# Kernel tuning notes

Measured on AMD Instinct MI355X. Metric: run time of the kernel, lower is better.

## Reference

```python
import jax, jax.numpy as jnp
import numpy as np

IN_CH, OUT_CH = 32, 32
MODES1, MODES2 = 16, 16
B, H, W = 16, 256, 256


def setup_inputs() -> dict:
    key = jax.random.key(0)
    k1, k2, k3 = jax.random.split(key, 3)
    scale = 1.0 / (IN_CH * OUT_CH)
    x = jax.random.normal(k1, (B, IN_CH, H, W), dtype=jnp.float32)
    # weights stored as real view of complex: [..., 2] = (real, imag)
    w1 = scale * jax.random.uniform(k2, (IN_CH, OUT_CH, MODES1, MODES2, 2), dtype=jnp.float32)
    w2 = scale * jax.random.uniform(k3, (IN_CH, OUT_CH, MODES1, MODES2, 2), dtype=jnp.float32)
    return {"x": x, "w1": w1, "w2": w2}


def reference(x, w1, w2):
    m1, m2 = MODES1, MODES2
    b, _, h, w = x.shape
    x_ft = jnp.fft.rfft2(x, axes=(-2, -1))  # [B, in_ch, H, W//2+1] complex
    c1 = w1[..., 0] + 1j * w1[..., 1]       # [in_ch, out_ch, m1, m2]
    c2 = w2[..., 0] + 1j * w2[..., 1]
    o1 = jnp.einsum('bixy,ioxy->boxy', x_ft[:, :, :m1, :m2], c1)
    o2 = jnp.einsum('bixy,ioxy->boxy', x_ft[:, :, -m1:, :m2], c2)
    out_ft = jnp.zeros((b, c1.shape[1], h, w // 2 + 1), dtype=x_ft.dtype)
    out_ft = out_ft.at[:, :, :m1, :m2].set(o1)
    out_ft = out_ft.at[:, :, -m1:, :m2].set(o2)
    return jnp.fft.irfft2(out_ft, s=(h, w), axes=(-2, -1))
```

## Files before the change

kernel.cpp:

```cpp
#include <hip/hip_runtime.h>
#include <math.h>

#define BB 16
#define CC 32
#define HH 256
#define WW 256
#define NIMG (BB * CC)

typedef _Float16 f16;
typedef __attribute__((ext_vector_type(8))) _Float16 f16x8;
typedef __attribute__((ext_vector_type(4))) float f32x4;

constexpr float TWO_PI_OVER_256 = 6.28318530717958647692f / 256.0f;

#define N_TWF 8192
#define N_ACOL 32768
#define N_AINV 16384
#define N_BINV 8192

static __device__ __forceinline__ f32x4 mfma3(f16x8 ah, f16x8 al, f16x8 bh,
                                              f16x8 bl, f32x4 c) {
  c = __builtin_amdgcn_mfma_f32_16x16x32_f16(ah, bh, c, 0, 0, 0);
  c = __builtin_amdgcn_mfma_f32_16x16x32_f16(ah, bl, c, 0, 0, 0);
  c = __builtin_amdgcn_mfma_f32_16x16x32_f16(al, bh, c, 0, 0, 0);
  return c;
}

static __device__ __forceinline__ void split16(float v, f16* hi, f16* lo) {
  f16 h_ = (f16)v;
  *hi = h_;
  *lo = (f16)(v - (float)h_);
}

__global__ __launch_bounds__(256) void k_tw(f16* __restrict__ fb) {
  const int id = blockIdx.x * 256 + threadIdx.x;
  f16* twf_hi = fb;
  f16* twf_lo = twf_hi + N_TWF;
  f16* acol_hi = twf_lo + N_TWF;
  f16* acol_lo = acol_hi + N_ACOL;
  f16* ainv_hi = acol_lo + N_ACOL;
  f16* ainv_lo = ainv_hi + N_AINV;
  f16* binv_hi = ainv_lo + N_AINV;
  f16* binv_lo = binv_hi + N_BINV;

  float v;
  f16 *dh, *dl;
  if (id < N_TWF) {
    int idx = id;
    int j = idx & 7, lane = (idx >> 3) & 63, ks = (idx >> 9) & 7,
        nt = (idx >> 12) & 1;
    int col = nt * 16 + (lane & 15);
    int w = ks * 32 + ((lane >> 4) << 3) + j;
    int kx = col >> 1, ri = col & 1;
    int ph = (kx * w) & 255;
    float s, c;
    sincosf(TWO_PI_OVER_256 * (float)ph, &s, &c);
    v = ri ? -s : c;
    dh = twf_hi + idx;
    dl = twf_lo + idx;
  } else if (id < N_TWF + N_ACOL) {
    int idx = id - N_TWF;
    int j = idx & 7, lane = (idx >> 3) & 63, ks = (idx >> 9) & 15,
        mt = (idx >> 13) & 3;
    int row = mt * 16 + (lane & 15);
    int k = ks * 32 + ((lane >> 4) << 3) + j;
    int h = k >> 1, rj = k & 1;
    int zr = (row < 32) ? row : row - 32;
    int ky = (zr < 16) ? zr : 224 + zr;
    int ph = (ky * h) & 255;
    float s, c;
    sincosf(TWO_PI_OVER_256 * (float)ph, &s, &c);
    if (row < 32)
      v = rj ? s : c;
    else
      v = rj ? c : -s;
    dh = acol_hi + idx;
    dl = acol_lo + idx;
  } else if (id < N_TWF + N_ACOL + N_AINV) {
    int idx = id - N_TWF - N_ACOL;
    int j = idx & 7, lane = (idx >> 3) & 63, ks = (idx >> 9) & 1,
        mt = (idx >> 10) & 15;
    int h = mt * 16 + (lane & 15);
    int k = ks * 32 + ((lane >> 4) << 3) + j;
    int zr = k >> 1, rj = k & 1;
    int ky = (zr < 16) ? zr : 224 + zr;
    int ph = (ky * h) & 255;
    float s, c;
    sincosf(TWO_PI_OVER_256 * (float)ph, &s, &c);
    v = rj ? s : c;
    dh = ainv_hi + idx;
    dl = ainv_lo + idx;
  } else {
    int idx = id - N_TWF - N_ACOL - N_AINV;
    int j = idx & 7, lane = (idx >> 3) & 63, nt = (idx >> 9) & 15;
    int w = nt * 16 + (lane & 15);
    int k = ((lane >> 4) << 3) + j;
    int kx = k >> 1, ri = k & 1;
    int ph = (kx * w) & 255;
    float s, c;
    sincosf(TWO_PI_OVER_256 * (float)ph, &s, &c);
    float scale = ((kx == 0) ? 1.0f : 2.0f) / 65536.0f;
    v = ri ? -scale * s : scale * c;
    dh = binv_hi + idx;
    dl = binv_lo + idx;
  }
  f16 hi, lo;
  split16(v, &hi, &lo);
  *dh = hi;
  *dl = lo;
}

__global__ __launch_bounds__(256) void k_fwd(const float* __restrict__ x,
                                             const f16* __restrict__ twf_hi,
                                             const f16* __restrict__ twf_lo,
                                             const f16* __restrict__ acol_hi,
                                             const f16* __restrict__ acol_lo,
                                             float* __restrict__ Z) {
  __shared__ __align__(16) f16 Yc_hi[16 * 520];
  __shared__ __align__(16) f16 Yc_lo[16 * 520];
  const int t = threadIdx.x, lane = t & 63, wid = t >> 6;
  const int l15 = lane & 15, kgrp = lane >> 4;
  const int img = blockIdx.x;
  const float* xim = x + (size_t)img * (HH * WW);

  for (int r = 0; r < 4; ++r) {
    const int mt = r * 4 + wid;
    f32x4 acc0 = {0.f, 0.f, 0.f, 0.f}, acc1 = {0.f, 0.f, 0.f, 0.f};
    const float* ap = xim + (mt * 16 + l15) * WW + kgrp * 8;
#pragma unroll
    for (int ks = 0; ks < 8; ++ks) {
      float4 v0 = *(const float4*)(ap + ks * 32);
      float4 v1 = *(const float4*)(ap + ks * 32 + 4);
      float vv[8] = {v0.x, v0.y, v0.z, v0.w, v1.x, v1.y, v1.z, v1.w};
      f16x8 ah, al;
#pragma unroll
      for (int e = 0; e < 8; ++e) {
        f16 h_ = (f16)vv[e];
        ah[e] = h_;
        al[e] = (f16)(vv[e] - (float)h_);
      }
      const int b0 = ((0 * 8 + ks) * 64 + lane) * 8;
      const int b1 = ((1 * 8 + ks) * 64 + lane) * 8;
      f16x8 b0h = *(const f16x8*)(twf_hi + b0);
      f16x8 b0l = *(const f16x8*)(twf_lo + b0);
      f16x8 b1h = *(const f16x8*)(twf_hi + b1);
      f16x8 b1l = *(const f16x8*)(twf_lo + b1);
      acc0 = mfma3(ah, al, b0h, b0l, acc0);
      acc1 = mfma3(ah, al, b1h, b1l, acc1);
    }
#pragma unroll
    for (int nt = 0; nt < 2; ++nt) {
#pragma unroll
      for (int jj = 0; jj < 4; ++jj) {
        const int h = mt * 16 + kgrp * 4 + jj;
        const int n = nt * 16 + l15;
        const int kx = n >> 1, ri = n & 1;
        float v = (nt == 0) ? acc0[jj] : acc1[jj];
        f16 hv = (f16)v;
        Yc_hi[kx * 520 + 2 * h + ri] = hv;
        Yc_lo[kx * 520 + 2 * h + ri] = (f16)(v - (float)hv);
      }
    }
  }
  __syncthreads();
  f32x4 zacc = {0.f, 0.f, 0.f, 0.f};
#pragma unroll 4
  for (int ks = 0; ks < 16; ++ks) {
    const int ao = ((wid * 16 + ks) * 64 + lane) * 8;
    f16x8 a_h = *(const f16x8*)(acol_hi + ao);
    f16x8 a_l = *(const f16x8*)(acol_lo + ao);
    const int bo = l15 * 520 + ks * 32 + kgrp * 8;
    f16x8 b_h = *(const f16x8*)(Yc_hi + bo);
    f16x8 b_l = *(const f16x8*)(Yc_lo + bo);
    zacc = mfma3(a_h, a_l, b_h, b_l, zacc);
  }
  float* zp = Z + (size_t)img * 1024;
#pragma unroll
  for (int jj = 0; jj < 4; ++jj) {
    const int row = wid * 16 + kgrp * 4 + jj;
    zp[row * 16 + l15] = zacc[jj];
  }
}

__global__ __launch_bounds__(256) void k_mix(const float* __restrict__ Z,
                                             const float* __restrict__ w1,
                                             const float* __restrict__ w2,
                                             float* __restrict__ O) {
  __shared__ float2 zs[BB][CC];
  __shared__ float2 cs[CC][CC];
  const int t = threadIdx.x;
  const int zr = blockIdx.x >> 4;
  const int kx = blockIdx.x & 15;
  const int kyi = zr & 15;
  const float* wsrc = (zr < 16) ? w1 : w2;
#pragma unroll
  for (int p = t; p < BB * CC; p += 256) {
    int b = p >> 5, i = p & 31;
    const float* zi = Z + (size_t)(b * CC + i) * 1024;
    zs[b][i] = make_float2(zi[zr * 16 + kx], zi[512 + zr * 16 + kx]);
  }
#pragma unroll
  for (int p = t; p < CC * CC; p += 256) {
    int i = p >> 5, oc = p & 31;
    const float* src = wsrc + ((size_t)((i * CC + oc) * 16 + kyi) * 16 + kx) * 2;
    cs[i][oc] = make_float2(src[0], src[1]);
  }
  __syncthreads();
  const int oc = t & 31;
  const int b0 = t >> 5;
#pragma unroll
  for (int pass = 0; pass < 2; ++pass) {
    const int b = b0 + pass * 8;
    float acc_r = 0.f, acc_i = 0.f;
#pragma unroll
    for (int i = 0; i < CC; ++i) {
      float2 zv = zs[b][i];
      float2 cv = cs[i][oc];
      acc_r += zv.x * cv.x - zv.y * cv.y;
      acc_i += zv.x * cv.y + zv.y * cv.x;
    }
    float2* dst = (float2*)O + (size_t)(b * CC + oc) * 512 + zr * 16 + kx;
    *dst = make_float2(acc_r, acc_i);
  }
}

__global__ __launch_bounds__(256) void k_inv(const float* __restrict__ O,
                                             const f16* __restrict__ ainv_hi,
                                             const f16* __restrict__ ainv_lo,
                                             const f16* __restrict__ binv_hi,
                                             const f16* __restrict__ binv_lo,
                                             float* __restrict__ out) {
  __shared__ float Olds[1024];
  __shared__ __align__(16) f16 Bf_hi[2048], Bf_lo[2048];
  __shared__ __align__(16) f16 T_hi[256 * 40], T_lo[256 * 40];
  const int t = threadIdx.x, lane = t & 63, wid = t >> 6;
  const int l15 = lane & 15, kgrp = lane >> 4;
  const int img = blockIdx.x;
  {
    float4 v = ((const float4*)(O + (size_t)img * 1024))[t];
    *(float4*)&Olds[t * 4] = v;
  }
  __syncthreads();
#pragma unroll
  for (int e = 0; e < 8; ++e) {
    const int idx = e * 256 + t;
    const int nt = idx >> 10, ks = (idx >> 9) & 1, ln = (idx >> 3) & 63,
              j = idx & 7;
    const int k = ks * 32 + ((ln >> 4) << 3) + j;
    const int n = nt * 16 + (ln & 15);
    const int zr = k >> 1, rj = k & 1, kx = n >> 1, ri = n & 1;
    const float Or = Olds[(zr * 16 + kx) * 2];
    const float Oi = Olds[(zr * 16 + kx) * 2 + 1];
    const float v = (rj == 0) ? (ri == 0 ? Or : Oi) : (ri == 0 ? -Oi : Or);
    f16 hv = (f16)v;
    Bf_hi[idx] = hv;
    Bf_lo[idx] = (f16)(v - (float)hv);
  }
  __syncthreads();
#pragma unroll
  for (int mm = 0; mm < 4; ++mm) {
    const int mt = wid * 4 + mm;
    f32x4 acc0 = {0.f, 0.f, 0.f, 0.f}, acc1 = {0.f, 0.f, 0.f, 0.f};
#pragma unroll
    for (int ks = 0; ks < 2; ++ks) {
      const int ao = ((mt * 2 + ks) * 64 + lane) * 8;
      f16x8 a_h = *(const f16x8*)(ainv_hi + ao);
      f16x8 a_l = *(const f16x8*)(ainv_lo + ao);
      const int bo0 = ((0 * 2 + ks) * 64 + lane) * 8;
      const int bo1 = ((1 * 2 + ks) * 64 + lane) * 8;
      f16x8 b0h = *(const f16x8*)(Bf_hi + bo0);
      f16x8 b0l = *(const f16x8*)(Bf_lo + bo0);
      f16x8 b1h = *(const f16x8*)(Bf_hi + bo1);
      f16x8 b1l = *(const f16x8*)(Bf_lo + bo1);
      acc0 = mfma3(a_h, a_l, b0h, b0l, acc0);
      acc1 = mfma3(a_h, a_l, b1h, b1l, acc1);
    }
#pragma unroll
    for (int nt = 0; nt < 2; ++nt) {
#pragma unroll
      for (int jj = 0; jj < 4; ++jj) {
        const int h = mt * 16 + kgrp * 4 + jj;
        const int n = nt * 16 + l15;
        float v = (nt == 0) ? acc0[jj] : acc1[jj];
        f16 hv = (f16)v;
        T_hi[h * 40 + n] = hv;
        T_lo[h * 40 + n] = (f16)(v - (float)hv);
      }
    }
  }
  __syncthreads();
  float* op = out + (size_t)img * (HH * WW);
#pragma unroll
  for (int mm = 0; mm < 4; ++mm) {
    const int mt = wid * 4 + mm;
    const int ao = (mt * 16 + l15) * 40 + kgrp * 8;
    f16x8 a_h = *(const f16x8*)(T_hi + ao);
    f16x8 a_l = *(const f16x8*)(T_lo + ao);
#pragma unroll 4
    for (int nt = 0; nt < 16; ++nt) {
      const int bo = (nt * 64 + lane) * 8;
      f16x8 b_h = *(const f16x8*)(binv_hi + bo);
      f16x8 b_l = *(const f16x8*)(binv_lo + bo);
      f32x4 acc = {0.f, 0.f, 0.f, 0.f};
      acc = mfma3(a_h, a_l, b_h, b_l, acc);
#pragma unroll
      for (int jj = 0; jj < 4; ++jj) {
        const int h = mt * 16 + kgrp * 4 + jj;
        op[(size_t)h * WW + nt * 16 + l15] = acc[jj];
      }
    }
  }
}

extern "C" void kernel_launch(void* const* d_in, const int* in_sizes, int n_in,
                              void* d_out, int out_size, void* d_ws,
                              size_t ws_size, hipStream_t stream) {
  const float* x = (const float*)d_in[0];
  const float* w1 = (const float*)d_in[1];
  const float* w2 = (const float*)d_in[2];
  float* out = (float*)d_out;

  f16* fb = (f16*)d_ws;
  f16* twf_hi = fb;
  f16* twf_lo = twf_hi + N_TWF;
  f16* acol_hi = twf_lo + N_TWF;
  f16* acol_lo = acol_hi + N_ACOL;
  f16* ainv_hi = acol_lo + N_ACOL;
  f16* ainv_lo = ainv_hi + N_AINV;
  f16* binv_hi = ainv_lo + N_AINV;
  f16* binv_lo = binv_hi + N_BINV;
  float* Z = (float*)(binv_lo + N_BINV);
  float* O = Z + (size_t)NIMG * 1024;

  k_tw<<<dim3(256), dim3(256), 0, stream>>>(fb);
  k_fwd<<<dim3(NIMG), dim3(256), 0, stream>>>(x, twf_hi, twf_lo, acol_hi,
                                              acol_lo, Z);
  k_mix<<<dim3(512), dim3(256), 0, stream>>>(Z, w1, w2, O);
  k_inv<<<dim3(NIMG), dim3(256), 0, stream>>>(O, ainv_hi, ainv_lo, binv_hi,
                                              binv_lo, out);
}
```

Measured before the change: 81.45 us.

## Split forward and inverse per-image work into two row-half blocks

Each image is now handled by two blocks, each covering 128 rows, in both the forward and inverse kernels, which doubles the grid to 1024 blocks. The forward kernel writes two partial column-DFT results per image, and the mix kernel sums them as it loads. The acol twiddle layout is reindexed so each half reads its own slice of rows. This targets low occupancy from only 512 large blocks on a GPU with many CUs, at the cost of extra partial-sum traffic and duplicated Bf construction in the inverse kernel.

Result: slower. 88.08 us (+8.1%).

```diff
diff --git a/kernel.cpp b/kernel.cpp
--- a/kernel.cpp
+++ b/kernel.cpp
@@ -60,11 +60,12 @@
     dl = twf_lo + idx;
   } else if (id < N_TWF + N_ACOL) {
     int idx = id - N_TWF;
-    int j = idx & 7, lane = (idx >> 3) & 63, ks = (idx >> 9) & 15,
-        mt = (idx >> 13) & 3;
+    int j = idx & 7, lane = (idx >> 3) & 63, ks = (idx >> 9) & 7,
+        mt = (idx >> 12) & 3, half = (idx >> 14) & 1;
     int row = mt * 16 + (lane & 15);
     int k = ks * 32 + ((lane >> 4) << 3) + j;
-    int h = k >> 1, rj = k & 1;
+    int h = half * 128 + (k >> 1);
+    int rj = k & 1;
     int zr = (row < 32) ? row : row - 32;
     int ky = (zr < 16) ? zr : 224 + zr;
     int ph = (ky * h) & 255;
@@ -115,15 +116,16 @@
                                              const f16* __restrict__ twf_lo,
                                              const f16* __restrict__ acol_hi,
                                              const f16* __restrict__ acol_lo,
-                                             float* __restrict__ Z) {
-  __shared__ __align__(16) f16 Yc_hi[16 * 520];
-  __shared__ __align__(16) f16 Yc_lo[16 * 520];
+                                             float* __restrict__ Zp) {
+  __shared__ __align__(16) f16 Yc_hi[16 * 260];
+  __shared__ __align__(16) f16 Yc_lo[16 * 260];
   const int t = threadIdx.x, lane = t & 63, wid = t >> 6;
   const int l15 = lane & 15, kgrp = lane >> 4;
-  const int img = blockIdx.x;
-  const float* xim = x + (size_t)img * (HH * WW);
-
-  for (int r = 0; r < 4; ++r) {
+  const int img = blockIdx.x >> 1;
+  const int half = blockIdx.x & 1;
+  const float* xim = x + (size_t)img * (HH * WW) + half * 128 * WW;
+
+  for (int r = 0; r < 2; ++r) {
     const int mt = r * 4 + wid;
     f32x4 acc0 = {0.f, 0.f, 0.f, 0.f}, acc1 = {0.f, 0.f, 0.f, 0.f};
     const float* ap = xim + (mt * 16 + l15) * WW + kgrp * 8;
@@ -152,29 +154,29 @@
     for (int nt = 0; nt < 2; ++nt) {
 #pragma unroll
       for (int jj = 0; jj < 4; ++jj) {
-        const int h = mt * 16 + kgrp * 4 + jj;
+        const int hl = mt * 16 + kgrp * 4 + jj;
         const int n = nt * 16 + l15;
         const int kx = n >> 1, ri = n & 1;
         float v = (nt == 0) ? acc0[jj] : acc1[jj];
         f16 hv = (f16)v;
-        Yc_hi[kx * 520 + 2 * h + ri] = hv;
-        Yc_lo[kx * 520 + 2 * h + ri] = (f16)(v - (float)hv);
+        Yc_hi[kx * 260 + 2 * hl + ri] = hv;
+        Yc_lo[kx * 260 + 2 * hl + ri] = (f16)(v - (float)hv);
       }
     }
   }
   __syncthreads();
   f32x4 zacc = {0.f, 0.f, 0.f, 0.f};
-#pragma unroll 4
-  for (int ks = 0; ks < 16; ++ks) {
-    const int ao = ((wid * 16 + ks) * 64 + lane) * 8;
+#pragma unroll
+  for (int ks = 0; ks < 8; ++ks) {
+    const int ao = ((((half * 4 + wid) * 8) + ks) * 64 + lane) * 8;
     f16x8 a_h = *(const f16x8*)(acol_hi + ao);
     f16x8 a_l = *(const f16x8*)(acol_lo + ao);
-    const int bo = l15 * 520 + ks * 32 + kgrp * 8;
+    const int bo = l15 * 260 + ks * 32 + kgrp * 8;
     f16x8 b_h = *(const f16x8*)(Yc_hi + bo);
     f16x8 b_l = *(const f16x8*)(Yc_lo + bo);
     zacc = mfma3(a_h, a_l, b_h, b_l, zacc);
   }
-  float* zp = Z + (size_t)img * 1024;
+  float* zp = Zp + ((size_t)img * 2 + half) * 1024;
 #pragma unroll
   for (int jj = 0; jj < 4; ++jj) {
     const int row = wid * 16 + kgrp * 4 + jj;
@@ -182,7 +184,7 @@
   }
 }
 
-__global__ __launch_bounds__(256) void k_mix(const float* __restrict__ Z,
+__global__ __launch_bounds__(256) void k_mix(const float* __restrict__ Zp,
                                              const float* __restrict__ w1,
                                              const float* __restrict__ w2,
                                              float* __restrict__ O) {
@@ -196,8 +198,10 @@
 #pragma unroll
   for (int p = t; p < BB * CC; p += 256) {
     int b = p >> 5, i = p & 31;
-    const float* zi = Z + (size_t)(b * CC + i) * 1024;
-    zs[b][i] = make_float2(zi[zr * 16 + kx], zi[512 + zr * 16 + kx]);
+    const float* zi = Zp + (size_t)(b * CC + i) * 2048;
+    float re = zi[zr * 16 + kx] + zi[1024 + zr * 16 + kx];
+    float im = zi[512 + zr * 16 + kx] + zi[1536 + zr * 16 + kx];
+    zs[b][i] = make_float2(re, im);
   }
 #pragma unroll
   for (int p = t; p < CC * CC; p += 256) {
@@ -232,10 +236,11 @@
                                              float* __restrict__ out) {
   __shared__ float Olds[1024];
   __shared__ __align__(16) f16 Bf_hi[2048], Bf_lo[2048];
-  __shared__ __align__(16) f16 T_hi[256 * 40], T_lo[256 * 40];
+  __shared__ __align__(16) f16 T_hi[128 * 40], T_lo[128 * 40];
   const int t = threadIdx.x, lane = t & 63, wid = t >> 6;
   const int l15 = lane & 15, kgrp = lane >> 4;
-  const int img = blockIdx.x;
+  const int img = blockIdx.x >> 1;
+  const int half = blockIdx.x & 1;
   {
     float4 v = ((const float4*)(O + (size_t)img * 1024))[t];
     *(float4*)&Olds[t * 4] = v;
@@ -258,8 +263,9 @@
   }
   __syncthreads();
 #pragma unroll
-  for (int mm = 0; mm < 4; ++mm) {
-    const int mt = wid * 4 + mm;
+  for (int mm = 0; mm < 2; ++mm) {
+    const int mtl = wid * 2 + mm;
+    const int mt = half * 8 + mtl;
     f32x4 acc0 = {0.f, 0.f, 0.f, 0.f}, acc1 = {0.f, 0.f, 0.f, 0.f};
 #pragma unroll
     for (int ks = 0; ks < 2; ++ks) {
@@ -279,21 +285,21 @@
     for (int nt = 0; nt < 2; ++nt) {
 #pragma unroll
       for (int jj = 0; jj < 4; ++jj) {
-        const int h = mt * 16 + kgrp * 4 + jj;
+        const int hl = mtl * 16 + kgrp * 4 + jj;
         const int n = nt * 16 + l15;
         float v = (nt == 0) ? acc0[jj] : acc1[jj];
         f16 hv = (f16)v;
-        T_hi[h * 40 + n] = hv;
-        T_lo[h * 40 + n] = (f16)(v - (float)hv);
+        T_hi[hl * 40 + n] = hv;
+        T_lo[hl * 40 + n] = (f16)(v - (float)hv);
       }
     }
   }
   __syncthreads();
-  float* op = out + (size_t)img * (HH * WW);
-#pragma unroll
-  for (int mm = 0; mm < 4; ++mm) {
-    const int mt = wid * 4 + mm;
-    const int ao = (mt * 16 + l15) * 40 + kgrp * 8;
+  float* op = out + (size_t)img * (HH * WW) + (size_t)half * 128 * WW;
+#pragma unroll
+  for (int mm = 0; mm < 2; ++mm) {
+    const int mtl = wid * 2 + mm;
+    const int ao = (mtl * 16 + l15) * 40 + kgrp * 8;
     f16x8 a_h = *(const f16x8*)(T_hi + ao);
     f16x8 a_l = *(const f16x8*)(T_lo + ao);
 #pragma unroll 4
@@ -305,8 +311,8 @@
       acc = mfma3(a_h, a_l, b_h, b_l, acc);
 #pragma unroll
       for (int jj = 0; jj < 4; ++jj) {
-        const int h = mt * 16 + kgrp * 4 + jj;
-        op[(size_t)h * WW + nt * 16 + l15] = acc[jj];
+        const int hl = mtl * 16 + kgrp * 4 + jj;
+        op[(size_t)hl * WW + nt * 16 + l15] = acc[jj];
       }
     }
   }
@@ -329,13 +335,13 @@
   f16* ainv_lo = ainv_hi + N_AINV;
   f16* binv_hi = ainv_lo + N_AINV;
   f16* binv_lo = binv_hi + N_BINV;
-  float* Z = (float*)(binv_lo + N_BINV);
-  float* O = Z + (size_t)NIMG * 1024;
+  float* Zp = (float*)(binv_lo + N_BINV);
+  float* O = Zp + (size_t)NIMG * 2048;
 
   k_tw<<<dim3(256), dim3(256), 0, stream>>>(fb);
-  k_fwd<<<dim3(NIMG), dim3(256), 0, stream>>>(x, twf_hi, twf_lo, acol_hi,
-                                              acol_lo, Z);
-  k_mix<<<dim3(512), dim3(256), 0, stream>>>(Z, w1, w2, O);
-  k_inv<<<dim3(NIMG), dim3(256), 0, stream>>>(O, ainv_hi, ainv_lo, binv_hi,
-                                              binv_lo, out);
-}
+  k_fwd<<<dim3(NIMG * 2), dim3(256), 0, stream>>>(x, twf_hi, twf_lo, acol_hi,
+                                                  acol_lo, Zp);
+  k_mix<<<dim3(512), dim3(256), 0, stream>>>(Zp, w1, w2, O);
+  k_inv<<<dim3(NIMG * 2), dim3(256), 0, stream>>>(O, ainv_hi, ainv_lo, binv_hi,
+                                                  binv_lo, out);
+}
```
